# Kernel tuning notes

Hardware: AMD Instinct MI355X
Metric: run time of the kernel (lower is better)

## Reference

```python
import jax, jax.numpy as jnp
import numpy as np

B, H1, H2, D, V1 = 4, 512, 640, 640, 1025  # V1 = vocab_size + 1 (blank)
T, U = 256, 128


def setup_inputs() -> dict:
    key = jax.random.key(0)
    ks = jax.random.split(key, 8)
    s = lambda fan_in: 1.0 / np.sqrt(fan_in)
    return {
        "encoder_outputs": jax.random.normal(ks[0], (B, H1, T), jnp.float32),
        "predictor_outputs": jax.random.normal(ks[1], (B, H2, U), jnp.float32),
        # Linear weights stored as [in, out]
        "W_enc": jax.random.uniform(ks[2], (H1, D), jnp.float32, -s(H1), s(H1)),
        "b_enc": jax.random.uniform(ks[3], (D,), jnp.float32, -s(H1), s(H1)),
        "W_pred": jax.random.uniform(ks[4], (H2, D), jnp.float32, -s(H2), s(H2)),
        "b_pred": jax.random.uniform(ks[5], (D,), jnp.float32, -s(H2), s(H2)),
        "W_out": jax.random.uniform(ks[6], (D, V1), jnp.float32, -s(D), s(D)),
        "b_out": jax.random.uniform(ks[7], (V1,), jnp.float32, -s(D), s(D)),
    }


def reference(encoder_outputs, predictor_outputs, W_enc, b_enc, W_pred, b_pred, W_out, b_out):
    # transpose(1,2): [B,H1,T] -> [B,T,H1], [B,H2,U] -> [B,U,H2], fused into einsum
    f = jnp.einsum("bht,hd->btd", encoder_outputs, W_enc) + b_enc   # [B,T,D]
    g = jnp.einsum("bhu,hd->bud", predictor_outputs, W_pred) + b_pred  # [B,U,D]
    h = jax.nn.relu(f[:, :, None, :] + g[:, None, :, :])            # [B,T,U,D]
    logits = jnp.einsum("btud,dv->btuv", h, W_out) + b_out          # [B,T,U,V+1]
    return jax.nn.log_softmax(logits, axis=-1)
```

## Files before the change

kernel.cpp:

```cpp
#include <hip/hip_runtime.h>
#include <hip/hip_bf16.h>

#define Bb 4
#define Tt 256
#define Uu 128
#define H1 512
#define H2 640
#define Dd 640
#define V1c 1025

typedef __bf16 bf16x8 __attribute__((ext_vector_type(8)));
typedef unsigned short ushort8 __attribute__((ext_vector_type(8)));
typedef unsigned short ushort4v __attribute__((ext_vector_type(4)));
typedef float floatx4 __attribute__((ext_vector_type(4)));

static __device__ __forceinline__ unsigned short f2bf(float x) {
    union { float f; unsigned u; } a; a.f = x;
    unsigned r = a.u + 0x7fffu + ((a.u >> 16) & 1u);
    return (unsigned short)(r >> 16);
}
static __device__ __forceinline__ float bf2f(unsigned short x) {
    union { unsigned u; float f; } a; a.u = ((unsigned)x) << 16; return a.f;
}

__global__ __launch_bounds__(640) void fg_fused(const float* __restrict__ enc,
                                                const float* __restrict__ Wenc,
                                                const float* __restrict__ benc,
                                                float* __restrict__ f,
                                                const float* __restrict__ pred,
                                                const float* __restrict__ Wpred,
                                                const float* __restrict__ bpred,
                                                float* __restrict__ g) {
    __shared__ float s[640 * 8];
    const bool isF = blockIdx.x < 128;
    const float* in   = isF ? enc : pred;
    const float* W    = isF ? Wenc : Wpred;
    const float* bias = isF ? benc : bpred;
    float* out        = isF ? f : g;
    const int H    = isF ? H1 : H2;
    const int Tdim = isF ? Tt : Uu;
    const int blk  = isF ? (int)blockIdx.x : (int)blockIdx.x - 128;
    const int tBlocks = Tdim >> 3;
    const int b  = blk / tBlocks;
    const int t0 = (blk % tBlocks) << 3;
    const float* inB = in + (size_t)b * H * Tdim + t0;
    const int tid = threadIdx.x;

    for (int h = tid; h < H; h += 640) {
        float4 v0 = *(const float4*)(inB + (size_t)h * Tdim);
        float4 v1 = *(const float4*)(inB + (size_t)h * Tdim + 4);
        *(float4*)(&s[h * 8])     = v0;
        *(float4*)(&s[h * 8 + 4]) = v1;
    }
    __syncthreads();

    const int d = tid;
    float acc[8];
    #pragma unroll
    for (int j = 0; j < 8; ++j) acc[j] = 0.f;
    #pragma unroll 4
    for (int h = 0; h < H; ++h) {
        float w = W[(size_t)h * Dd + d];
        float4 s0 = *(const float4*)(&s[h * 8]);
        float4 s1 = *(const float4*)(&s[h * 8 + 4]);
        acc[0] += s0.x * w; acc[1] += s0.y * w; acc[2] += s0.z * w; acc[3] += s0.w * w;
        acc[4] += s1.x * w; acc[5] += s1.y * w; acc[6] += s1.z * w; acc[7] += s1.w * w;
    }
    float bv = bias[d];
    float* o = out + ((size_t)b * Tdim + t0) * Dd + d;
    #pragma unroll
    for (int j = 0; j < 8; ++j) o[(size_t)j * Dd] = acc[j] + bv;
}

__global__ __launch_bounds__(256) void conv_wout2(const float* __restrict__ Wout,
                                                  unsigned short* __restrict__ Wb2,
                                                  float* __restrict__ wtail) {
    __shared__ float tile[32][128];
    const int blk = blockIdx.x;
    const int w = blk / 20;
    const int db = blk % 20;
    const int tid = threadIdx.x;

    #pragma unroll
    for (int i = 0; i < 16; ++i) {
        int idx = tid + 256 * i;
        int d_loc = idx >> 7;
        int v_loc = idx & 127;
        tile[d_loc][v_loc] = Wout[(size_t)(db * 32 + d_loc) * V1c + w * 128 + v_loc];
    }
    __syncthreads();

    #pragma unroll
    for (int k = 0; k < 2; ++k) {
        int gidx = tid * 2 + k;
        int nt  = gidx >> 6;
        int rem = gidx & 63;
        int l15 = rem >> 2;
        int lg  = rem & 3;
        int v_loc = nt * 16 + l15;
        ushort8 pk;
        #pragma unroll
        for (int j = 0; j < 8; ++j) pk[j] = f2bf(tile[lg * 8 + j][v_loc]);
        *(ushort8*)(Wb2 + (size_t)w * 81920 + db * 4096 + gidx * 8) = pk;
    }

    if (blk == 0) {
        for (int dd = tid; dd < Dd; dd += 256) wtail[dd] = Wout[(size_t)dd * V1c + 1024];
    }
}

__global__ __launch_bounds__(512, 2) void joint_main(const float* __restrict__ f,
                                                     const float* __restrict__ g,
                                                     const unsigned short* __restrict__ Wb2,
                                                     const float* __restrict__ wtail,
                                                     const float* __restrict__ b_out,
                                                     float* __restrict__ out) {
    __shared__ __align__(16) union UU {
        struct { unsigned short hlds[64 * 328]; float wtld[640]; } a;
        float sOut[8 * 1025];
    } u;
    __shared__ float sPart[8 * 64];
    __shared__ float sRed[64];
    __shared__ float sTail[64];

    const int tid = threadIdx.x;
    const int l = tid & 63;
    const int w = tid >> 6;
    const int l15 = l & 15;
    const int lg = l >> 4;

    const int blk = blockIdx.x;
    const int uhalf = blk & 1;
    const int t = (blk >> 1) & 255;
    const int b = blk >> 9;
    const int u0 = uhalf * 64;
    const size_t fbase = ((size_t)b * Tt + t) * Dd;
    const size_t gbase = ((size_t)b * Uu + u0) * Dd;
    const size_t rowbase = (size_t)(b * Tt + t) * Uu + u0;

    for (int i = tid; i < Dd; i += 512) u.a.wtld[i] = wtail[i];

    floatx4 acc[4][8];
    #pragma unroll
    for (int i = 0; i < 4; ++i)
        #pragma unroll
        for (int j = 0; j < 8; ++j) acc[i][j] = (floatx4){0.f, 0.f, 0.f, 0.f};

    const unsigned short* __restrict__ bbase = Wb2 + (size_t)w * 81920 + (l15 * 32 + lg * 8);
    float tailAcc = 0.f;
    const int srow = w * 8 + (l >> 3);
    const int ssub = l & 7;

    for (int half = 0; half < 2; ++half) {
        const int dhb = half * 320;
        __syncthreads();
        {
            const int row = tid >> 3;
            #pragma unroll
            for (int j = 0; j < 10; ++j) {
                int c4 = (tid & 7) + 8 * j;
                int d = dhb + c4 * 4;
                float4 fv = *(const float4*)(f + fbase + d);
                float4 gv = *(const float4*)(g + gbase + (size_t)row * Dd + d);
                float h0 = fv.x + gv.x; h0 = h0 > 0.f ? h0 : 0.f;
                float h1 = fv.y + gv.y; h1 = h1 > 0.f ? h1 : 0.f;
                float h2 = fv.z + gv.z; h2 = h2 > 0.f ? h2 : 0.f;
                float h3 = fv.w + gv.w; h3 = h3 > 0.f ? h3 : 0.f;
                ushort4v pk;
                pk.x = f2bf(h0); pk.y = f2bf(h1); pk.z = f2bf(h2); pk.w = f2bf(h3);
                *(ushort4v*)(&u.a.hlds[row * 328 + c4 * 4]) = pk;
            }
        }
        __syncthreads();

        ushort8 Bbuf[2][8];
        {
            const int ksg0 = half * 10;
            #pragma unroll
            for (int nt = 0; nt < 8; ++nt)
                Bbuf[0][nt] = *(const ushort8*)(bbase + ksg0 * 4096 + nt * 512);
        }
        #pragma unroll
        for (int ks = 0; ks < 10; ++ks) {
            const int ksg = half * 10 + ks;
            if (ks < 9) {
                #pragma unroll
                for (int nt = 0; nt < 8; ++nt)
                    Bbuf[(ks + 1) & 1][nt] =
                        *(const ushort8*)(bbase + (ksg + 1) * 4096 + nt * 512);
            }
            bf16x8 afrag[4];
            #pragma unroll
            for (int mt = 0; mt < 4; ++mt) {
                ushort8 av = *(const ushort8*)(&u.a.hlds[(mt * 16 + l15) * 328 + ks * 32 + lg * 8]);
                afrag[mt] = __builtin_bit_cast(bf16x8, av);
            }
            #pragma unroll
            for (int nt = 0; nt < 8; ++nt) {
                bf16x8 bfrag = __builtin_bit_cast(bf16x8, Bbuf[ks & 1][nt]);
                #pragma unroll
                for (int mt = 0; mt < 4; ++mt) {
                    acc[mt][nt] = __builtin_amdgcn_mfma_f32_16x16x32_bf16(
                        afrag[mt], bfrag, acc[mt][nt], 0, 0, 0);
                }
            }
        }

        #pragma unroll
        for (int j = 0; j < 10; ++j) {
            int c4 = ssub + 8 * j;
            ushort4v hv = *(const ushort4v*)(&u.a.hlds[srow * 328 + c4 * 4]);
            float4 wv = *(const float4*)(&u.a.wtld[dhb + c4 * 4]);
            tailAcc += bf2f(hv.x) * wv.x + bf2f(hv.y) * wv.y +
                       bf2f(hv.z) * wv.z + bf2f(hv.w) * wv.w;
        }
    }

    tailAcc += __shfl_xor(tailAcc, 1);
    tailAcc += __shfl_xor(tailAcc, 2);
    tailAcc += __shfl_xor(tailAcc, 4);
    if (ssub == 0) sTail[srow] = tailAcc + b_out[1024];

    #pragma unroll
    for (int nt = 0; nt < 8; ++nt) {
        float bo = b_out[w * 128 + nt * 16 + l15];
        #pragma unroll
        for (int mt = 0; mt < 4; ++mt)
            #pragma unroll
            for (int r = 0; r < 4; ++r) acc[mt][nt][r] += bo;
    }

    #pragma unroll
    for (int mt = 0; mt < 4; ++mt) {
        #pragma unroll
        for (int r = 0; r < 4; ++r) {
            float m = acc[mt][0][r];
            #pragma unroll
            for (int nt = 1; nt < 8; ++nt) m = fmaxf(m, acc[mt][nt][r]);
            #pragma unroll
            for (int msk = 1; msk < 16; msk <<= 1) m = fmaxf(m, __shfl_xor(m, msk));
            if (l15 == 0) sPart[w * 64 + mt * 16 + lg * 4 + r] = m;
        }
    }
    __syncthreads();
    if (tid < 64) {
        float m = sTail[tid];
        #pragma unroll
        for (int ww = 0; ww < 8; ++ww) m = fmaxf(m, sPart[ww * 64 + tid]);
        sRed[tid] = m;
    }
    __syncthreads();

    #pragma unroll
    for (int mt = 0; mt < 4; ++mt) {
        #pragma unroll
        for (int r = 0; r < 4; ++r) {
            int row = mt * 16 + lg * 4 + r;
            float mx = sRed[row];
            float sv = 0.f;
            #pragma unroll
            for (int nt = 0; nt < 8; ++nt) sv += __expf(acc[mt][nt][r] - mx);
            #pragma unroll
            for (int msk = 1; msk < 16; msk <<= 1) sv += __shfl_xor(sv, msk);
            if (l15 == 0) sPart[w * 64 + row] = sv;
        }
    }
    __syncthreads();
    if (tid < 64) {
        float mx = sRed[tid];
        float sv = __expf(sTail[tid] - mx);
        #pragma unroll
        for (int ww = 0; ww < 8; ++ww) sv += sPart[ww * 64 + tid];
        sRed[tid] = mx + logf(sv);
    }
    __syncthreads();

    for (int grp = 0; grp < 8; ++grp) {
        const int mt = grp >> 1;
        const int half8 = grp & 1;
        if ((lg >> 1) == half8) {
            const int row_local = (lg & 1) * 4;
            #pragma unroll
            for (int nt = 0; nt < 8; ++nt) {
                #pragma unroll
                for (int r = 0; r < 4; ++r) {
                    u.sOut[(row_local + r) * 1025 + w * 128 + nt * 16 + l15] =
                        acc[mt][nt][r] - sRed[grp * 8 + row_local + r];
                }
            }
        }
        if (tid < 8) u.sOut[tid * 1025 + 1024] = sTail[grp * 8 + tid] - sRed[grp * 8 + tid];
        __syncthreads();
        float* outp = out + (rowbase + grp * 8) * (size_t)V1c;
        #pragma unroll
        for (int k = 0; k < 4; ++k) {
            int i4 = tid + 512 * k;
            floatx4 v = *(const floatx4*)(&u.sOut[4 * i4]);
            __builtin_nontemporal_store(v, (floatx4*)(outp + 4 * i4));
        }
        if (tid < 2) {
            int i4 = tid + 2048;
            floatx4 v = *(const floatx4*)(&u.sOut[4 * i4]);
            __builtin_nontemporal_store(v, (floatx4*)(outp + 4 * i4));
        }
        __syncthreads();
    }
}

extern "C" void kernel_launch(void* const* d_in, const int* in_sizes, int n_in,
                              void* d_out, int out_size, void* d_ws, size_t ws_size,
                              hipStream_t stream) {
    const float* enc   = (const float*)d_in[0];
    const float* pred  = (const float*)d_in[1];
    const float* Wenc  = (const float*)d_in[2];
    const float* benc  = (const float*)d_in[3];
    const float* Wpred = (const float*)d_in[4];
    const float* bpred = (const float*)d_in[5];
    const float* Wout  = (const float*)d_in[6];
    const float* bout  = (const float*)d_in[7];

    float* f = (float*)d_ws;
    float* g = f + (size_t)Bb * Tt * Dd;
    unsigned short* Wb2 = (unsigned short*)(g + (size_t)Bb * Uu * Dd);
    float* wtail = (float*)(Wb2 + 8 * 81920);

    fg_fused<<<192, 640, 0, stream>>>(enc, Wenc, benc, f, pred, Wpred, bpred, g);
    conv_wout2<<<160, 256, 0, stream>>>(Wout, Wb2, wtail);
    joint_main<<<Bb * Tt * 2, 512, 0, stream>>>(f, g, Wb2, wtail, bout, (float*)d_out);
}
```

Before: 447.2 us.

## Stage full-depth activation tile in LDS and write output in 16-row groups

The joint kernel now builds the whole 640-wide ReLU(f+g) bf16 tile in shared memory up front, instead of two 320-wide halves. This removes a barrier pair and lets the MFMA loop run across all 20 k-steps without a break. The output epilogue now stages 16 rows per group instead of 8, which halves the number of barrier-separated store rounds and removes the lane-group predication. Shared memory roughly doubles to about 82KB per block, which may cut the two-blocks-per-CU occupancy set by launch bounds.

New measurement: 366.7 us. 18.0% less time.

```diff
diff --git a/kernel.cpp b/kernel.cpp
--- a/kernel.cpp
+++ b/kernel.cpp
@@ -116,9 +116,10 @@
                                                      const float* __restrict__ b_out,
                                                      float* __restrict__ out) {
     __shared__ __align__(16) union UU {
-        struct { unsigned short hlds[64 * 328]; float wtld[640]; } a;
-        float sOut[8 * 1025];
+        unsigned short hlds[2 * 64 * 328];
+        float sOut[16 * 1025];
     } u;
+    __shared__ float wtld[640];
     __shared__ float sPart[8 * 64];
     __shared__ float sRed[64];
     __shared__ float sTail[64];
@@ -138,7 +139,7 @@
     const size_t gbase = ((size_t)b * Uu + u0) * Dd;
     const size_t rowbase = (size_t)(b * Tt + t) * Uu + u0;
 
-    for (int i = tid; i < Dd; i += 512) u.a.wtld[i] = wtail[i];
+    for (int i = tid; i < Dd; i += 512) wtld[i] = wtail[i];
 
     floatx4 acc[4][8];
     #pragma unroll
@@ -151,53 +152,53 @@
     const int srow = w * 8 + (l >> 3);
     const int ssub = l & 7;
 
-    for (int half = 0; half < 2; ++half) {
-        const int dhb = half * 320;
-        __syncthreads();
-        {
-            const int row = tid >> 3;
-            #pragma unroll
-            for (int j = 0; j < 10; ++j) {
-                int c4 = (tid & 7) + 8 * j;
-                int d = dhb + c4 * 4;
-                float4 fv = *(const float4*)(f + fbase + d);
-                float4 gv = *(const float4*)(g + gbase + (size_t)row * Dd + d);
-                float h0 = fv.x + gv.x; h0 = h0 > 0.f ? h0 : 0.f;
-                float h1 = fv.y + gv.y; h1 = h1 > 0.f ? h1 : 0.f;
-                float h2 = fv.z + gv.z; h2 = h2 > 0.f ? h2 : 0.f;
-                float h3 = fv.w + gv.w; h3 = h3 > 0.f ? h3 : 0.f;
-                ushort4v pk;
-                pk.x = f2bf(h0); pk.y = f2bf(h1); pk.z = f2bf(h2); pk.w = f2bf(h3);
-                *(ushort4v*)(&u.a.hlds[row * 328 + c4 * 4]) = pk;
-            }
-        }
-        __syncthreads();
-
+    {
+        const int row = tid >> 3;
+        const float* frow = f + fbase;
+        const float* grow = g + gbase + (size_t)row * Dd;
+        #pragma unroll
+        for (int j = 0; j < 20; ++j) {
+            int c4 = (tid & 7) + 8 * j;
+            int d = c4 * 4;
+            int half = (j >= 10) ? 1 : 0;
+            int cloc = c4 - half * 80;
+            float4 fv = *(const float4*)(frow + d);
+            float4 gv = *(const float4*)(grow + d);
+            float h0 = fv.x + gv.x; h0 = h0 > 0.f ? h0 : 0.f;
+            float h1 = fv.y + gv.y; h1 = h1 > 0.f ? h1 : 0.f;
+            float h2 = fv.z + gv.z; h2 = h2 > 0.f ? h2 : 0.f;
+            float h3 = fv.w + gv.w; h3 = h3 > 0.f ? h3 : 0.f;
+            ushort4v pk;
+            pk.x = f2bf(h0); pk.y = f2bf(h1); pk.z = f2bf(h2); pk.w = f2bf(h3);
+            *(ushort4v*)(&u.hlds[half * 20992 + row * 328 + cloc * 4]) = pk;
+        }
+    }
+    __syncthreads();
+
+    {
         ushort8 Bbuf[2][8];
-        {
-            const int ksg0 = half * 10;
-            #pragma unroll
-            for (int nt = 0; nt < 8; ++nt)
-                Bbuf[0][nt] = *(const ushort8*)(bbase + ksg0 * 4096 + nt * 512);
-        }
-        #pragma unroll
-        for (int ks = 0; ks < 10; ++ks) {
-            const int ksg = half * 10 + ks;
-            if (ks < 9) {
+        #pragma unroll
+        for (int nt = 0; nt < 8; ++nt)
+            Bbuf[0][nt] = *(const ushort8*)(bbase + nt * 512);
+        #pragma unroll
+        for (int ksg = 0; ksg < 20; ++ksg) {
+            if (ksg < 19) {
                 #pragma unroll
                 for (int nt = 0; nt < 8; ++nt)
-                    Bbuf[(ks + 1) & 1][nt] =
+                    Bbuf[(ksg + 1) & 1][nt] =
                         *(const ushort8*)(bbase + (ksg + 1) * 4096 + nt * 512);
             }
+            const int bufo = (ksg >= 10) ? 20992 : 0;
+            const int ks = (ksg >= 10) ? (ksg - 10) : ksg;
             bf16x8 afrag[4];
             #pragma unroll
             for (int mt = 0; mt < 4; ++mt) {
-                ushort8 av = *(const ushort8*)(&u.a.hlds[(mt * 16 + l15) * 328 + ks * 32 + lg * 8]);
+                ushort8 av = *(const ushort8*)(&u.hlds[bufo + (mt * 16 + l15) * 328 + ks * 32 + lg * 8]);
                 afrag[mt] = __builtin_bit_cast(bf16x8, av);
             }
             #pragma unroll
             for (int nt = 0; nt < 8; ++nt) {
-                bf16x8 bfrag = __builtin_bit_cast(bf16x8, Bbuf[ks & 1][nt]);
+                bf16x8 bfrag = __builtin_bit_cast(bf16x8, Bbuf[ksg & 1][nt]);
                 #pragma unroll
                 for (int mt = 0; mt < 4; ++mt) {
                     acc[mt][nt] = __builtin_amdgcn_mfma_f32_16x16x32_bf16(
@@ -205,15 +206,17 @@
                 }
             }
         }
-
-        #pragma unroll
-        for (int j = 0; j < 10; ++j) {
-            int c4 = ssub + 8 * j;
-            ushort4v hv = *(const ushort4v*)(&u.a.hlds[srow * 328 + c4 * 4]);
-            float4 wv = *(const float4*)(&u.a.wtld[dhb + c4 * 4]);
-            tailAcc += bf2f(hv.x) * wv.x + bf2f(hv.y) * wv.y +
-                       bf2f(hv.z) * wv.z + bf2f(hv.w) * wv.w;
-        }
+    }
+
+    #pragma unroll
+    for (int j = 0; j < 20; ++j) {
+        int c4 = ssub + 8 * j;
+        int half = (j >= 10) ? 1 : 0;
+        int cloc = c4 - half * 80;
+        ushort4v hv = *(const ushort4v*)(&u.hlds[half * 20992 + srow * 328 + cloc * 4]);
+        float4 wv = *(const float4*)(&wtld[c4 * 4]);
+        tailAcc += bf2f(hv.x) * wv.x + bf2f(hv.y) * wv.y +
+                   bf2f(hv.z) * wv.z + bf2f(hv.w) * wv.w;
     }
 
     tailAcc += __shfl_xor(tailAcc, 1);
@@ -275,31 +278,27 @@
     }
     __syncthreads();
 
-    for (int grp = 0; grp < 8; ++grp) {
-        const int mt = grp >> 1;
-        const int half8 = grp & 1;
-        if ((lg >> 1) == half8) {
-            const int row_local = (lg & 1) * 4;
-            #pragma unroll
-            for (int nt = 0; nt < 8; ++nt) {
-                #pragma unroll
-                for (int r = 0; r < 4; ++r) {
-                    u.sOut[(row_local + r) * 1025 + w * 128 + nt * 16 + l15] =
-                        acc[mt][nt][r] - sRed[grp * 8 + row_local + r];
-                }
+    #pragma unroll
+    for (int grp = 0; grp < 4; ++grp) {
+        #pragma unroll
+        for (int nt = 0; nt < 8; ++nt) {
+            #pragma unroll
+            for (int r = 0; r < 4; ++r) {
+                u.sOut[(lg * 4 + r) * 1025 + w * 128 + nt * 16 + l15] =
+                    acc[grp][nt][r] - sRed[grp * 16 + lg * 4 + r];
             }
         }
-        if (tid < 8) u.sOut[tid * 1025 + 1024] = sTail[grp * 8 + tid] - sRed[grp * 8 + tid];
+        if (tid < 16) u.sOut[tid * 1025 + 1024] = sTail[grp * 16 + tid] - sRed[grp * 16 + tid];
         __syncthreads();
-        float* outp = out + (rowbase + grp * 8) * (size_t)V1c;
-        #pragma unroll
-        for (int k = 0; k < 4; ++k) {
+        float* outp = out + (rowbase + grp * 16) * (size_t)V1c;
+        #pragma unroll
+        for (int k = 0; k < 8; ++k) {
             int i4 = tid + 512 * k;
             floatx4 v = *(const floatx4*)(&u.sOut[4 * i4]);
             __builtin_nontemporal_store(v, (floatx4*)(outp + 4 * i4));
         }
-        if (tid < 2) {
-            int i4 = tid + 2048;
+        if (tid < 4) {
+            int i4 = tid + 4096;
             floatx4 v = *(const floatx4*)(&u.sOut[4 * i4]);
             __builtin_nontemporal_store(v, (floatx4*)(outp + 4 * i4));
         }
```
